# Performance work log

Hardware: AMD Instinct MI355X
Metric: run time of the kernel (lower is better)

Reference implementation:

```python
import jax, jax.numpy as jnp
import numpy as np

B, C, D = 512, 50000, 256
N_LOADED = 40000


def setup_inputs() -> dict:
    key = jax.random.key(0)
    k1, k2, k3, k4 = jax.random.split(key, 4)
    visual_feats = jax.random.normal(k1, (B, D), dtype=jnp.float32)
    text_feats = jax.random.normal(k2, (C, D), dtype=jnp.float32)
    # sparse multi-hot labels; force class 0 positive for every row so the
    # positive set (intersected with loaded ids) is never empty
    batch_label = (jax.random.uniform(k3, (B, C)) < 0.02).astype(jnp.int32)
    batch_label = batch_label.at[:, 0].set(1)
    # distinct loaded class ids; force id 0 to be loaded
    ids = jax.random.permutation(k4, C)[:N_LOADED].astype(jnp.int32)
    ids = jnp.sort(ids).at[0].set(0)
    return {
        "visual_feats": visual_feats,
        "text_feats": text_feats,
        "batch_label": batch_label,
        "class_ids_loaded": ids,
        "d_space": D,
    }


def reference(visual_feats, text_feats, batch_label, class_ids_loaded, d_space):
    num_classes = text_feats.shape[0]
    # membership mask for loaded class ids (the set() intersection in torch)
    loaded = jnp.zeros((num_classes,), dtype=bool).at[class_ids_loaded].set(True)

    # cosine similarity; note: torch adds 1e-6 eps only to text-feature norms
    v = visual_feats / jnp.linalg.norm(visual_feats, axis=1, keepdims=True)
    t = text_feats / (1e-6 + jnp.linalg.norm(text_feats, axis=1, keepdims=True))
    S = v @ t.T  # [B, C]

    pos = (batch_label != 0) & loaded[None, :]  # ragged positive sets, as mask
    neg = (batch_label == 0) & loaded[None, :]  # ragged negative sets, as mask

    # denominator: sum of exp(sim) over negatives, per row
    denom = jnp.sum(jnp.where(neg, jnp.exp(S), 0.0), axis=1)  # [B]
    n_pos = jnp.sum(pos, axis=1).astype(S.dtype)  # [B]

    # per-row loss: mean over positives of -log(exp(s_p)/denom) = log(denom)-s_p
    per_row = jnp.sum(jnp.where(pos, jnp.log(denom)[:, None] - S, 0.0), axis=1) / n_pos
    return jnp.mean(per_row).reshape(1)
```

## Files before the change

kernel.cpp:

```cpp
#include <hip/hip_runtime.h>
#include <math.h>

#define D_DIM 256
#define TM 128
#define TN 128
#define BK 32

typedef __attribute__((ext_vector_type(8))) short short8;
typedef __attribute__((ext_vector_type(4))) float floatx4;
typedef unsigned long long u64;

__device__ __forceinline__ unsigned short f2bf(float f) {
    unsigned int u = __float_as_uint(f);
    u += 0x7FFFu + ((u >> 16) & 1u);
    return (unsigned short)(u >> 16);
}

__device__ __forceinline__ void gload16(const void* g, void* lds) {
    __builtin_amdgcn_global_load_lds(
        (const __attribute__((address_space(1))) unsigned int*)g,
        (__attribute__((address_space(3))) unsigned int*)lds, 16, 0, 0);
}

__global__ void init_zero(u64* lm, int nwords) {
    int i = blockIdx.x * blockDim.x + threadIdx.x;
    if (i < nwords) lm[i] = 0ull;
}

__global__ void prep(const float* __restrict__ V, const float* __restrict__ T,
                     const int* __restrict__ ids, u64* __restrict__ loadedmask,
                     unsigned short* __restrict__ Vb, unsigned short* __restrict__ Tb,
                     int B, int C, int n_loaded) {
    int gtid = blockIdx.x * blockDim.x + threadIdx.x;
    if (gtid < n_loaded) {
        int id = ids[gtid];
        atomicOr(&loadedmask[id >> 6], 1ull << (id & 63));
    }
    int wave = gtid >> 6;
    int lane = threadIdx.x & 63;
    if (wave >= B + C) return;
    bool isV = wave < B;
    const float* src = isV ? (V + (size_t)wave * D_DIM)
                           : (T + (size_t)(wave - B) * D_DIM);
    float4 x = ((const float4*)src)[lane];
    float ss = x.x * x.x + x.y * x.y + x.z * x.z + x.w * x.w;
    #pragma unroll
    for (int off = 32; off > 0; off >>= 1) ss += __shfl_xor(ss, off);
    float nrm = sqrtf(ss);
    float s = isV ? (1.0f / nrm) : (1.0f / (1e-6f + nrm));
    ushort4 o;
    o.x = f2bf(x.x * s); o.y = f2bf(x.y * s);
    o.z = f2bf(x.z * s); o.w = f2bf(x.w * s);
    unsigned short* dst = isV ? (Vb + (size_t)wave * D_DIM)
                              : (Tb + (size_t)(wave - B) * D_DIM);
    ((ushort4*)dst)[lane] = o;
}

__global__ __launch_bounds__(256) void gemm_fused(
    const unsigned short* __restrict__ Vb, const unsigned short* __restrict__ Tb,
    const int* __restrict__ label, const u64* __restrict__ loadedmask,
    float* __restrict__ denomP, float* __restrict__ posP, float* __restrict__ npP,
    int C) {
    __shared__ unsigned short As[TM * BK];
    __shared__ unsigned short Bs[TN * BK];
    __shared__ unsigned char  Lab[TM * TN];
    __shared__ float sDen[TM], sPos[TM], sNp[TM];

    const int tid  = threadIdx.x;
    const int lane = tid & 63;
    const int w    = tid >> 6;
    const int m0 = blockIdx.x * TM;
    const int n0 = blockIdx.y * TN;

    if (tid < TM) { sDen[tid] = 0.f; sPos[tid] = 0.f; sNp[tid] = 0.f; }

    if (n0 + TN <= C) {
        #pragma unroll
        for (int j = 0; j < 16; ++j) {
            int idx = j * 256 + tid;
            int r  = idx >> 5;
            int c4 = idx & 31;
            int4 v = *(const int4*)(label + (size_t)(m0 + r) * C + n0 + c4 * 4);
            unsigned int p = (v.x ? 1u : 0u) | (v.y ? 0x100u : 0u) |
                             (v.z ? 0x10000u : 0u) | (v.w ? 0x1000000u : 0u);
            *(unsigned int*)&Lab[r * TN + c4 * 4] = p;
        }
    } else {
        for (int j = 0; j < 16; ++j) {
            int idx = j * 256 + tid;
            int r  = idx >> 5;
            int c4 = idx & 31;
            const int* lp = label + (size_t)(m0 + r) * C;
            unsigned int p = 0;
            #pragma unroll
            for (int e = 0; e < 4; ++e) {
                int c = n0 + c4 * 4 + e;
                if (c < C && lp[c]) p |= 1u << (8 * e);
            }
            *(unsigned int*)&Lab[r * TN + c4 * 4] = p;
        }
    }

    const int sra = lane >> 2;
    const int kc  = (lane & 3) * 8;
    int ga = m0 + w * 32 + sra;
    int gb0 = n0 + w * 32 + sra;
    int gb1 = gb0 + 16;
    if (gb0 >= C) gb0 = C - 1;
    if (gb1 >= C) gb1 = C - 1;
    const unsigned short* gA0 = Vb + (size_t)ga * D_DIM + kc;
    const unsigned short* gA1 = gA0 + (size_t)16 * D_DIM;
    const unsigned short* gB0 = Tb + (size_t)gb0 * D_DIM + kc;
    const unsigned short* gB1 = Tb + (size_t)gb1 * D_DIM + kc;
    unsigned short* lA0 = &As[w * 32 * BK];
    unsigned short* lA1 = lA0 + 16 * BK;
    unsigned short* lB0 = &Bs[w * 32 * BK];
    unsigned short* lB1 = lB0 + 16 * BK;

    const int wm = (w >> 1) * 64;
    const int wn = (w & 1) * 64;
    const int fr = lane & 15;
    const int quad = lane >> 4;

    floatx4 acc[4][4];
    #pragma unroll
    for (int mi = 0; mi < 4; mi++)
        #pragma unroll
        for (int ni = 0; ni < 4; ni++) acc[mi][ni] = (floatx4)0.f;

    #pragma unroll
    for (int kt = 0; kt < D_DIM / BK; ++kt) {
        if (kt) __syncthreads();
        const int kb = kt * BK;
        gload16(gA0 + kb, lA0);
        gload16(gA1 + kb, lA1);
        gload16(gB0 + kb, lB0);
        gload16(gB1 + kb, lB1);
        __syncthreads();
        short8 af[4], bf[4];
        #pragma unroll
        for (int mi = 0; mi < 4; mi++)
            af[mi] = *(const short8*)&As[(wm + mi * 16 + fr) * BK + quad * 8];
        #pragma unroll
        for (int ni = 0; ni < 4; ni++)
            bf[ni] = *(const short8*)&Bs[(wn + ni * 16 + fr) * BK + quad * 8];
        #pragma unroll
        for (int mi = 0; mi < 4; mi++)
            #pragma unroll
            for (int ni = 0; ni < 4; ni++)
                acc[mi][ni] = __builtin_amdgcn_mfma_f32_16x16x32_bf16(
                    af[mi], bf[ni], acc[mi][ni], 0, 0, 0);
    }

    const u64 loadedw = loadedmask[(n0 + wn) >> 6];
    #pragma unroll
    for (int mi = 0; mi < 4; mi++) {
        #pragma unroll
        for (int i = 0; i < 4; i++) {
            const int mloc = wm + mi * 16 + quad * 4 + i;
            float den = 0.f, pos = 0.f, np = 0.f;
            #pragma unroll
            for (int ni = 0; ni < 4; ni++) {
                const int nloc = wn + ni * 16 + fr;
                const int bit  = ni * 16 + fr;
                const float s = acc[mi][ni][i];
                const int lab = Lab[mloc * TN + nloc];
                if ((loadedw >> bit) & 1) {
                    if (lab) { pos += s; np += 1.f; }
                    else     { den += __expf(s); }
                }
            }
            #pragma unroll
            for (int off = 8; off >= 1; off >>= 1) {
                den += __shfl_xor(den, off);
                pos += __shfl_xor(pos, off);
                np  += __shfl_xor(np, off);
            }
            if (fr == 0) {
                if (den != 0.f) atomicAdd(&sDen[mloc], den);
                if (np  != 0.f) { atomicAdd(&sPos[mloc], pos); atomicAdd(&sNp[mloc], np); }
            }
        }
    }
    __syncthreads();
    if (tid < TM) {
        size_t idx = (size_t)blockIdx.y * 512 + m0 + tid;
        denomP[idx] = sDen[tid];
        posP[idx]   = sPos[tid];
        npP[idx]    = sNp[tid];
    }
}

__global__ void reduce_rows(const float* __restrict__ denomP, const float* __restrict__ posP,
                            const float* __restrict__ npP, float* __restrict__ pr,
                            int B, int NB) {
    int row  = blockIdx.x * 4 + (threadIdx.x >> 6);
    int lane = threadIdx.x & 63;
    if (row >= B) return;
    float den = 0.f, pos = 0.f, np = 0.f;
    for (int bn = lane; bn < NB; bn += 64) {
        den += denomP[(size_t)bn * B + row];
        pos += posP[(size_t)bn * B + row];
        np  += npP[(size_t)bn * B + row];
    }
    #pragma unroll
    for (int off = 32; off > 0; off >>= 1) {
        den += __shfl_xor(den, off);
        pos += __shfl_xor(pos, off);
        np  += __shfl_xor(np, off);
    }
    if (lane == 0) pr[row] = logf(den) - pos / np;
}

__global__ void final_mean(const float* __restrict__ pr, float* __restrict__ out, int B) {
    __shared__ float red[512];
    int tid = threadIdx.x;
    red[tid] = (tid < B) ? pr[tid] : 0.f;
    __syncthreads();
    for (int s = 256; s > 0; s >>= 1) {
        if (tid < s) red[tid] += red[tid + s];
        __syncthreads();
    }
    if (tid == 0) out[0] = red[0] / (float)B;
}

extern "C" void kernel_launch(void* const* d_in, const int* in_sizes, int n_in,
                              void* d_out, int out_size, void* d_ws, size_t ws_size,
                              hipStream_t stream) {
    const float* V     = (const float*)d_in[0];
    const float* T     = (const float*)d_in[1];
    const int*   label = (const int*)d_in[2];
    const int*   ids   = (const int*)d_in[3];
    int B = in_sizes[0] / D_DIM;
    int C = in_sizes[1] / D_DIM;
    int n_loaded = in_sizes[3];
    int WPR = (C + 63) >> 6;
    int NB  = (C + TN - 1) / TN;

    char* ws = (char*)d_ws;
    float* pr      = (float*)(ws + 0);
    u64*   loadedmask = (u64*)(ws + 2048);
    unsigned short* Vb = (unsigned short*)(ws + 8320);
    unsigned short* Tb = (unsigned short*)(ws + 270464);
    float* denomP  = (float*)(ws + 25870464);
    float* posP    = (float*)(ws + 26671232);
    float* npP     = (float*)(ws + 27472000);

    init_zero<<<(WPR + 255) / 256, 256, 0, stream>>>(loadedmask, WPR);

    int threads_needed = (B + C) * 64;
    prep<<<(threads_needed + 255) / 256, 256, 0, stream>>>(
        V, T, ids, loadedmask, Vb, Tb, B, C, n_loaded);

    dim3 grid(B / TM, NB);
    gemm_fused<<<grid, 256, 0, stream>>>(Vb, Tb, label, loadedmask,
                                         denomP, posP, npP, C);

    reduce_rows<<<(B + 3) / 4, 256, 0, stream>>>(denomP, posP, npP, pr, B, NB);

    final_mean<<<1, 512, 0, stream>>>(pr, (float*)d_out, B);
}
```

Measured before the change: 264.9 us.

## Compress labels to per-row bitmasks before GEMM and build loaded mask without atomics

Adds a compress kernel that turns the int32 label matrix into 64-bit positive bitmasks per row, already ANDed with the loaded mask. The GEMM epilogue reads those bitmasks instead of staging a byte label tile in LDS, and positive counts move to popcounts in the row reduction. The loaded mask is now built by a binary search over the sorted ids, which removes the init kernel and the atomics. The partial sums switch to a row-major layout with a fixed stride. The full label matrix is still read once, now by a separate kernel, which adds a launch. The binary search relies on the ids being sorted.

```diff
diff --git a/kernel.cpp b/kernel.cpp
--- a/kernel.cpp
+++ b/kernel.cpp
@@ -5,6 +5,7 @@
 #define TM 128
 #define TN 128
 #define BK 32
+#define NBP 392
 
 typedef __attribute__((ext_vector_type(8))) short short8;
 typedef __attribute__((ext_vector_type(4))) float floatx4;
@@ -22,19 +23,21 @@
         (__attribute__((address_space(3))) unsigned int*)lds, 16, 0, 0);
 }
 
-__global__ void init_zero(u64* lm, int nwords) {
-    int i = blockIdx.x * blockDim.x + threadIdx.x;
-    if (i < nwords) lm[i] = 0ull;
-}
-
 __global__ void prep(const float* __restrict__ V, const float* __restrict__ T,
                      const int* __restrict__ ids, u64* __restrict__ loadedmask,
                      unsigned short* __restrict__ Vb, unsigned short* __restrict__ Tb,
-                     int B, int C, int n_loaded) {
+                     int B, int C, int n_loaded, int WPR) {
     int gtid = blockIdx.x * blockDim.x + threadIdx.x;
-    if (gtid < n_loaded) {
-        int id = ids[gtid];
-        atomicOr(&loadedmask[id >> 6], 1ull << (id & 63));
+    if (gtid < WPR) {
+        int base = gtid << 6;
+        int lo = 0, hi = n_loaded;
+        while (lo < hi) { int mid = (lo + hi) >> 1; if (ids[mid] < base) lo = mid + 1; else hi = mid; }
+        u64 m = 0;
+        for (int i = lo; i < n_loaded; ++i) {
+            int v = ids[i]; if (v >= base + 64) break;
+            m |= 1ull << (v - base);
+        }
+        loadedmask[gtid] = m;
     }
     int wave = gtid >> 6;
     int lane = threadIdx.x & 63;
@@ -56,15 +59,38 @@
     ((ushort4*)dst)[lane] = o;
 }
 
+__global__ void compress(const int* __restrict__ label, const u64* __restrict__ loadedmask,
+                         u64* __restrict__ posmask, int C, int WPR) {
+    int row  = blockIdx.y;
+    int wir  = blockIdx.x * 4 + (threadIdx.x >> 6);
+    int lane = threadIdx.x & 63;
+    int w0   = wir * 16;
+    if (w0 >= WPR) return;
+    const int* lp = label + (size_t)row * C;
+    int lab[16];
+    #pragma unroll
+    for (int j = 0; j < 16; ++j) {
+        int wc  = w0 + j;
+        int col = (wc << 6) | lane;
+        lab[j] = (wc < WPR && col < C) ? lp[col] : 0;
+    }
+    #pragma unroll
+    for (int j = 0; j < 16; ++j) {
+        int wc = w0 + j;
+        if (wc < WPR) {
+            u64 posw = __ballot(lab[j] != 0) & loadedmask[wc];
+            if (lane == 0) posmask[(size_t)row * WPR + wc] = posw;
+        }
+    }
+}
+
 __global__ __launch_bounds__(256) void gemm_fused(
     const unsigned short* __restrict__ Vb, const unsigned short* __restrict__ Tb,
-    const int* __restrict__ label, const u64* __restrict__ loadedmask,
-    float* __restrict__ denomP, float* __restrict__ posP, float* __restrict__ npP,
-    int C) {
+    const u64* __restrict__ posmask, const u64* __restrict__ loadedmask,
+    float* __restrict__ denomP, float* __restrict__ posP, int C, int WPR) {
     __shared__ unsigned short As[TM * BK];
     __shared__ unsigned short Bs[TN * BK];
-    __shared__ unsigned char  Lab[TM * TN];
-    __shared__ float sDen[TM], sPos[TM], sNp[TM];
+    __shared__ float sDen[TM], sPos[TM];
 
     const int tid  = threadIdx.x;
     const int lane = tid & 63;
@@ -72,38 +98,11 @@
     const int m0 = blockIdx.x * TM;
     const int n0 = blockIdx.y * TN;
 
-    if (tid < TM) { sDen[tid] = 0.f; sPos[tid] = 0.f; sNp[tid] = 0.f; }
-
-    if (n0 + TN <= C) {
-        #pragma unroll
-        for (int j = 0; j < 16; ++j) {
-            int idx = j * 256 + tid;
-            int r  = idx >> 5;
-            int c4 = idx & 31;
-            int4 v = *(const int4*)(label + (size_t)(m0 + r) * C + n0 + c4 * 4);
-            unsigned int p = (v.x ? 1u : 0u) | (v.y ? 0x100u : 0u) |
-                             (v.z ? 0x10000u : 0u) | (v.w ? 0x1000000u : 0u);
-            *(unsigned int*)&Lab[r * TN + c4 * 4] = p;
-        }
-    } else {
-        for (int j = 0; j < 16; ++j) {
-            int idx = j * 256 + tid;
-            int r  = idx >> 5;
-            int c4 = idx & 31;
-            const int* lp = label + (size_t)(m0 + r) * C;
-            unsigned int p = 0;
-            #pragma unroll
-            for (int e = 0; e < 4; ++e) {
-                int c = n0 + c4 * 4 + e;
-                if (c < C && lp[c]) p |= 1u << (8 * e);
-            }
-            *(unsigned int*)&Lab[r * TN + c4 * 4] = p;
-        }
-    }
+    if (tid < TM) { sDen[tid] = 0.f; sPos[tid] = 0.f; }
 
     const int sra = lane >> 2;
     const int kc  = (lane & 3) * 8;
-    int ga = m0 + w * 32 + sra;
+    int ga  = m0 + w * 32 + sra;
     int gb0 = n0 + w * 32 + sra;
     int gb1 = gb0 + 16;
     if (gb0 >= C) gb0 = C - 1;
@@ -152,64 +151,62 @@
                     af[mi], bf[ni], acc[mi][ni], 0, 0, 0);
     }
 
-    const u64 loadedw = loadedmask[(n0 + wn) >> 6];
+    const int wcol = (n0 + wn) >> 6;
+    const u64 loadedw = loadedmask[wcol];
     #pragma unroll
     for (int mi = 0; mi < 4; mi++) {
         #pragma unroll
         for (int i = 0; i < 4; i++) {
             const int mloc = wm + mi * 16 + quad * 4 + i;
-            float den = 0.f, pos = 0.f, np = 0.f;
+            const u64 posw = posmask[(size_t)(m0 + mloc) * WPR + wcol];
+            const u64 negw = loadedw & ~posw;
+            float den = 0.f, pos = 0.f;
             #pragma unroll
             for (int ni = 0; ni < 4; ni++) {
-                const int nloc = wn + ni * 16 + fr;
-                const int bit  = ni * 16 + fr;
                 const float s = acc[mi][ni][i];
-                const int lab = Lab[mloc * TN + nloc];
-                if ((loadedw >> bit) & 1) {
-                    if (lab) { pos += s; np += 1.f; }
-                    else     { den += __expf(s); }
-                }
+                const int bit = ni * 16 + fr;
+                if ((negw >> bit) & 1) den += __expf(s);
+                if ((posw >> bit) & 1) pos += s;
             }
             #pragma unroll
             for (int off = 8; off >= 1; off >>= 1) {
                 den += __shfl_xor(den, off);
                 pos += __shfl_xor(pos, off);
-                np  += __shfl_xor(np, off);
             }
             if (fr == 0) {
                 if (den != 0.f) atomicAdd(&sDen[mloc], den);
-                if (np  != 0.f) { atomicAdd(&sPos[mloc], pos); atomicAdd(&sNp[mloc], np); }
+                if (pos != 0.f) atomicAdd(&sPos[mloc], pos);
             }
         }
     }
     __syncthreads();
     if (tid < TM) {
-        size_t idx = (size_t)blockIdx.y * 512 + m0 + tid;
-        denomP[idx] = sDen[tid];
-        posP[idx]   = sPos[tid];
-        npP[idx]    = sNp[tid];
+        denomP[(size_t)(m0 + tid) * NBP + blockIdx.y] = sDen[tid];
+        posP[(size_t)(m0 + tid) * NBP + blockIdx.y]   = sPos[tid];
     }
 }
 
 __global__ void reduce_rows(const float* __restrict__ denomP, const float* __restrict__ posP,
-                            const float* __restrict__ npP, float* __restrict__ pr,
-                            int B, int NB) {
+                            const u64* __restrict__ posmask, float* __restrict__ pr,
+                            int B, int NB, int WPR) {
     int row  = blockIdx.x * 4 + (threadIdx.x >> 6);
     int lane = threadIdx.x & 63;
     if (row >= B) return;
-    float den = 0.f, pos = 0.f, np = 0.f;
+    float den = 0.f, pos = 0.f;
     for (int bn = lane; bn < NB; bn += 64) {
-        den += denomP[(size_t)bn * B + row];
-        pos += posP[(size_t)bn * B + row];
-        np  += npP[(size_t)bn * B + row];
-    }
+        den += denomP[(size_t)row * NBP + bn];
+        pos += posP[(size_t)row * NBP + bn];
+    }
+    int cnt = 0;
+    for (int j = lane; j < WPR; j += 64)
+        cnt += __popcll(posmask[(size_t)row * WPR + j]);
     #pragma unroll
     for (int off = 32; off > 0; off >>= 1) {
         den += __shfl_xor(den, off);
         pos += __shfl_xor(pos, off);
-        np  += __shfl_xor(np, off);
-    }
-    if (lane == 0) pr[row] = logf(den) - pos / np;
+        cnt += __shfl_xor(cnt, off);
+    }
+    if (lane == 0) pr[row] = logf(den) - pos / (float)cnt;
 }
 
 __global__ void final_mean(const float* __restrict__ pr, float* __restrict__ out, int B) {
@@ -240,23 +237,25 @@
     char* ws = (char*)d_ws;
     float* pr      = (float*)(ws + 0);
     u64*   loadedmask = (u64*)(ws + 2048);
-    unsigned short* Vb = (unsigned short*)(ws + 8320);
-    unsigned short* Tb = (unsigned short*)(ws + 270464);
-    float* denomP  = (float*)(ws + 25870464);
-    float* posP    = (float*)(ws + 26671232);
-    float* npP     = (float*)(ws + 27472000);
-
-    init_zero<<<(WPR + 255) / 256, 256, 0, stream>>>(loadedmask, WPR);
+    u64*   posmask    = (u64*)(ws + 8320);
+    unsigned short* Vb = (unsigned short*)(ws + 3211392);
+    unsigned short* Tb = (unsigned short*)(ws + 3473536);
+    float* denomP  = (float*)(ws + 29073536);
+    float* posP    = (float*)(ws + 29876352);
 
     int threads_needed = (B + C) * 64;
     prep<<<(threads_needed + 255) / 256, 256, 0, stream>>>(
-        V, T, ids, loadedmask, Vb, Tb, B, C, n_loaded);
+        V, T, ids, loadedmask, Vb, Tb, B, C, n_loaded, WPR);
+
+    int wavesPerRow = (WPR + 15) / 16;
+    dim3 cgrid((wavesPerRow + 3) / 4, B);
+    compress<<<cgrid, 256, 0, stream>>>(label, loadedmask, posmask, C, WPR);
 
     dim3 grid(B / TM, NB);
-    gemm_fused<<<grid, 256, 0, stream>>>(Vb, Tb, label, loadedmask,
-                                         denomP, posP, npP, C);
-
-    reduce_rows<<<(B + 3) / 4, 256, 0, stream>>>(denomP, posP, npP, pr, B, NB);
+    gemm_fused<<<grid, 256, 0, stream>>>(Vb, Tb, posmask, loadedmask,
+                                         denomP, posP, C, WPR);
+
+    reduce_rows<<<(B + 3) / 4, 256, 0, stream>>>(denomP, posP, posmask, pr, B, NB, WPR);
 
     final_mean<<<1, 512, 0, stream>>>(pr, (float*)d_out, B);
 }
```

Result: slower. 305.2 us (+15.2%).
